# Kernel tuning notes

Hardware: AMD Instinct MI355X
Metric: run time of the kernel (lower is better)

Reference implementation:

```python
import jax, jax.numpy as jnp
import numpy as np

HEAD = 64            # RWKV_HEAD_SIZE
C = 1024             # n_embd = dim_att
F = 4096             # dim_ffn
B, T = 8, 256
H = C // HEAD
N_LAYER, LAYER_ID = 12, 1
GN_EPS = 1e-5 * 8 ** 2   # GroupNorm eps = 1e-5 * head_size_divisor^2


def bshift(x):
    """bidirectional_shift_multihead: per head, first half of channels shifted
    forward in time (right), second half shifted backward (left), zero-padded."""
    b, t, c = x.shape
    x4 = x.reshape(b, t, c // HEAD, HEAD)
    mid = HEAD // 2
    f = jnp.pad(x4[:, :-1, :, :mid], ((0, 0), (1, 0), (0, 0), (0, 0)))
    r = jnp.pad(x4[:, 1:, :, mid:], ((0, 0), (0, 1), (0, 0), (0, 0)))
    return jnp.concatenate([f, r], -1).reshape(b, t, c)


def layernorm(x, g, b):
    m = jnp.mean(x, -1, keepdims=True)
    v = jnp.mean((x - m) ** 2, -1, keepdims=True)
    return (x - m) * jax.lax.rsqrt(v + 1e-5) * g + b


def groupnorm(x, g, b):
    bb, t, c = x.shape
    xg = x.reshape(bb, t, H, HEAD)
    m = jnp.mean(xg, -1, keepdims=True)
    v = jnp.mean((xg - m) ** 2, -1, keepdims=True)
    return ((xg - m) * jax.lax.rsqrt(v + GN_EPS)).reshape(bb, t, c) * g + b


def wkv6_bi(r, k, v, w, u):
    """Bidirectional WKV6. r,k,v,w: [B,T,H,N]; u: [H,N].
    y_t = r_t . (S^fwd_t + u*k_t v_t^T + S^bwd_t), with per-channel decay
    d_t = exp(-exp(w_t)) applied to the state after each step in each direction."""
    d = jnp.exp(-jnp.exp(w))
    rT, kT, vT, dT = (jnp.moveaxis(a, 1, 0) for a in (r, k, v, d))  # [T,B,H,N]
    S0 = jnp.zeros((B, H, HEAD, HEAD), r.dtype)
    uB = u[None]  # [1,H,N]

    def fstep(S, inp):
        rt, kt, vt, dt = inp
        kv = kt[..., None] * vt[..., None, :]              # [B,H,N,N]
        y = jnp.einsum('bhj,bhji->bhi', rt, S + uB[..., None] * kv)
        return dt[..., None] * S + kv, y

    _, yf = jax.lax.scan(fstep, S0, (rT, kT, vT, dT))

    def bstep(S, inp):
        rt, kt, vt, dt = inp
        y = jnp.einsum('bhj,bhji->bhi', rt, S)
        return dt[..., None] * S + kt[..., None] * vt[..., None, :], y

    _, yb = jax.lax.scan(bstep, S0, (rT, kT, vT, dT), reverse=True)
    return jnp.moveaxis(yf + yb, 0, 1)  # [B,T,H,N]


def block_forward(x, ln1_g, ln1_b, ln2_g, ln2_b,
                  maa_x, maa_w, maa_k, maa_v, maa_r, maa_g, maa_w1, maa_w2,
                  time_decay, tdw1, tdw2, u, Wr, Wk, Wv, Wg, Wo, lnx_g, lnx_b,
                  cmaa_k, cmaa_r, Wck, Wcv, Wcr):
    # ---- RWKV_Tmix_V6 (attention) branch ----
    xa = layernorm(x, ln1_g, ln1_b)
    xx = bshift(xa) - xa
    a = jnp.tanh((xa + xx * maa_x) @ maa_w1).reshape(B, T, 5, -1)   # [B,T,5,32]
    m = jnp.einsum('btfd,fdc->fbtc', a, maa_w2)                      # [5,B,T,C]
    xw = xa + xx * (maa_w + m[0])
    xk = xa + xx * (maa_k + m[1])
    xv = xa + xx * (maa_v + m[2])
    xr = xa + xx * (maa_r + m[3])
    xg = xa + xx * (maa_g + m[4])
    r = (xr @ Wr).reshape(B, T, H, HEAD)
    k = (xk @ Wk).reshape(B, T, H, HEAD)
    v = (xv @ Wv).reshape(B, T, H, HEAD)
    g = jax.nn.silu(xg @ Wg)
    w = (time_decay + jnp.tanh(xw @ tdw1) @ tdw2).reshape(B, T, H, HEAD)
    y = wkv6_bi(r, k, v, w, u).reshape(B, T, C)
    y = groupnorm(y, lnx_g, lnx_b)
    x = x + (y * g) @ Wo
    # ---- RWKV_CMix_V6 (FFN) branch ----
    xc = layernorm(x, ln2_g, ln2_b)
    cxx = bshift(xc) - xc
    kk = jnp.square(jax.nn.relu((xc + cxx * cmaa_k) @ Wck))
    kv = kk @ Wcv
    x = x + jax.nn.sigmoid((xc + cxx * cmaa_r) @ Wcr) * kv
    return x


def setup_inputs() -> dict:
    key = jax.random.key(0)
    ks = jax.random.split(key, 16)
    r1 = 1.0 - LAYER_ID / N_LAYER            # ratio_1_to_almost0
    r0 = LAYER_ID / (N_LAYER - 1)            # ratio_0_to_1
    ddd = np.arange(C, dtype=np.float64) / C
    base = (1.0 - ddd ** r1).astype(np.float32)
    half = (1.0 - ddd ** (0.5 * r1)).astype(np.float32)
    s = 0.02
    p = {}
    p['x'] = jax.random.normal(ks[0], (B, T, C), jnp.float32)
    p['ln1_g'] = jnp.ones((C,), jnp.float32)
    p['ln1_b'] = jnp.zeros((C,), jnp.float32)
    p['ln2_g'] = jnp.ones((C,), jnp.float32)
    p['ln2_b'] = jnp.zeros((C,), jnp.float32)
    p['maa_x'] = jnp.asarray(base)
    p['maa_w'] = jnp.asarray(base)
    p['maa_k'] = jnp.asarray(base)
    p['maa_v'] = jnp.asarray((1.0 - (ddd ** r1 + 0.3 * r0)).astype(np.float32))
    p['maa_r'] = jnp.asarray(half)
    p['maa_g'] = jnp.asarray(half)
    p['maa_w1'] = jax.random.uniform(ks[1], (C, 160), jnp.float32, -0.01, 0.01)
    p['maa_w2'] = jax.random.uniform(ks[2], (5, 32, C), jnp.float32, -0.01, 0.01)
    n = np.arange(C, dtype=np.float64)
    p['time_decay'] = jnp.asarray((-6.0 + 5.0 * (n / (C - 1)) ** (0.7 + 1.3 * r0)).astype(np.float32))
    p['tdw1'] = jax.random.uniform(ks[3], (C, 64), jnp.float32, -0.01, 0.01)
    p['tdw2'] = jax.random.uniform(ks[4], (64, C), jnp.float32, -0.01, 0.01)
    faaaa = r0 * (1.0 - n / (C - 1)) + ((n + 1) % 3 - 1) * 0.1
    p['u'] = jnp.asarray(faaaa.reshape(H, HEAD).astype(np.float32))
    p['Wr'] = jax.random.normal(ks[5], (C, C), jnp.float32) * s
    p['Wk'] = jax.random.normal(ks[6], (C, C), jnp.float32) * s
    p['Wv'] = jax.random.normal(ks[7], (C, C), jnp.float32) * s
    p['Wg'] = jax.random.normal(ks[8], (C, C), jnp.float32) * s
    p['Wo'] = jax.random.normal(ks[9], (C, C), jnp.float32) * s
    p['lnx_g'] = jnp.ones((C,), jnp.float32)
    p['lnx_b'] = jnp.zeros((C,), jnp.float32)
    p['cmaa_k'] = jnp.asarray(base)
    p['cmaa_r'] = jnp.asarray(base)
    p['Wck'] = jax.random.normal(ks[10], (C, F), jnp.float32) * s
    p['Wcv'] = jax.random.normal(ks[11], (F, C), jnp.float32) * s
    p['Wcr'] = jax.random.normal(ks[12], (C, C), jnp.float32) * s
    return p


def reference(x, ln1_g, ln1_b, ln2_g, ln2_b,
              maa_x, maa_w, maa_k, maa_v, maa_r, maa_g, maa_w1, maa_w2,
              time_decay, tdw1, tdw2, u, Wr, Wk, Wv, Wg, Wo, lnx_g, lnx_b,
              cmaa_k, cmaa_r, Wck, Wcv, Wcr):
    return block_forward(x, ln1_g, ln1_b, ln2_g, ln2_b,
                         maa_x, maa_w, maa_k, maa_v, maa_r, maa_g, maa_w1, maa_w2,
                         time_decay, tdw1, tdw2, u, Wr, Wk, Wv, Wg, Wo, lnx_g, lnx_b,
                         cmaa_k, cmaa_r, Wck, Wcv, Wcr)
```

## Files before the change

### kernel.cpp

```cpp
#include <hip/hip_runtime.h>
#include <math.h>
#include <stdint.h>

static constexpr int B  = 8;
static constexpr int T  = 256;
static constexpr int C  = 1024;
static constexpr int H  = 16;
static constexpr int HEAD = 64;
static constexpr int FF = 4096;
static constexpr int BT = B * T;
static constexpr int NCH = 8;
static constexpr int CS  = 32;

typedef short short8  __attribute__((ext_vector_type(8)));
typedef float floatx4 __attribute__((ext_vector_type(4)));

__device__ __forceinline__ float bf2f(ushort u) {
    return __uint_as_float(((uint32_t)u) << 16);
}
__device__ __forceinline__ ushort f2bf(float x) {
    uint32_t u = __float_as_uint(x);
    u += 0x7fff + ((u >> 16) & 1);
    return (ushort)(u >> 16);
}

__device__ __forceinline__ void gload16(const void* g, void* l) {
    __builtin_amdgcn_global_load_lds(
        (const __attribute__((address_space(1))) unsigned int*)g,
        (__attribute__((address_space(3))) unsigned int*)l, 16, 0, 0);
}

#define BEPI_NONE_BF   0
#define BEPI_SILU_BF   1
#define BEPI_RELUSQ_BF 2
#define BEPI_NONE_F    3
#define BEPI_RES_F     4
#define BEPI_SIGRES_F  5
#define BEPI_TANH_F    6
#define BEPI_TANH_BF   7
#define BEPI_DECAY_F   8
#define BEPI_SIGRES2_F 9

__global__ __launch_bounds__(256) void ln_kernel(const float* __restrict__ x,
                                                 const float* __restrict__ g,
                                                 const float* __restrict__ b,
                                                 float* __restrict__ out)
{
    const int row = blockIdx.x;
    const int tid = threadIdx.x;
    const float4 v = reinterpret_cast<const float4*>(x + (size_t)row * C)[tid];
    float s = v.x + v.y + v.z + v.w;
#pragma unroll
    for (int off = 32; off > 0; off >>= 1) s += __shfl_xor(s, off);
    __shared__ float red[8];
    const int wave = tid >> 6, lane = tid & 63;
    if (lane == 0) red[wave] = s;
    __syncthreads();
    const float mean = (red[0] + red[1] + red[2] + red[3]) * (1.0f / C);
    const float d0 = v.x - mean, d1 = v.y - mean, d2 = v.z - mean, d3 = v.w - mean;
    float q = d0 * d0 + d1 * d1 + d2 * d2 + d3 * d3;
#pragma unroll
    for (int off = 32; off > 0; off >>= 1) q += __shfl_xor(q, off);
    if (lane == 0) red[4 + wave] = q;
    __syncthreads();
    const float var = (red[4] + red[5] + red[6] + red[7]) * (1.0f / C);
    const float rstd = rsqrtf(var + 1e-5f);
    const int c = tid * 4;
    float4 o;
    o.x = d0 * rstd * g[c + 0] + b[c + 0];
    o.y = d1 * rstd * g[c + 1] + b[c + 1];
    o.z = d2 * rstd * g[c + 2] + b[c + 2];
    o.w = d3 * rstd * g[c + 3] + b[c + 3];
    reinterpret_cast<float4*>(out + (size_t)row * C)[tid] = o;
}

__global__ __launch_bounds__(256) void bshiftmix_kernel(const float* __restrict__ xa,
                                                        const float* __restrict__ maa,
                                                        float* __restrict__ xx,
                                                        ushort* __restrict__ ax)
{
    const int i = blockIdx.x * 256 + threadIdx.x;
    const int c = i & (C - 1);
    const int bt = i >> 10;
    const int t = bt & (T - 1);
    const int j = c & (HEAD - 1);
    float src = 0.f;
    if (j < HEAD / 2) { if (t > 0)     src = xa[i - C]; }
    else              { if (t < T - 1) src = xa[i + C]; }
    const float a = xa[i];
    const float xv = src - a;
    xx[i] = xv;
    ax[i] = f2bf(a + xv * maa[c]);
}

__global__ __launch_bounds__(256) void bshiftcmix_kernel(const float* __restrict__ xc,
                                                         const float* __restrict__ mk,
                                                         const float* __restrict__ mr,
                                                         ushort* __restrict__ ok,
                                                         ushort* __restrict__ orr)
{
    const int i = blockIdx.x * 256 + threadIdx.x;
    const int c = i & (C - 1);
    const int bt = i >> 10;
    const int t = bt & (T - 1);
    const int j = c & (HEAD - 1);
    float src = 0.f;
    if (j < HEAD / 2) { if (t > 0)     src = xc[i - C]; }
    else              { if (t < T - 1) src = xc[i + C]; }
    const float a = xc[i];
    const float cxx = src - a;
    ok[i]  = f2bf(a + cxx * mk[c]);
    orr[i] = f2bf(a + cxx * mr[c]);
}

__global__ __launch_bounds__(1024) void gnmul_kernel(const float* __restrict__ yf,
                                                     const float* __restrict__ yb,
                                                     const float* __restrict__ g,
                                                     const float* __restrict__ b,
                                                     const ushort* __restrict__ gate,
                                                     const ushort* __restrict__ vin,
                                                     const ushort* __restrict__ rbuf,
                                                     const ushort* __restrict__ kbuf,
                                                     const float* __restrict__ u,
                                                     ushort* __restrict__ out)
{
    const int row = blockIdx.x;
    const int tid = threadIdx.x;
    const size_t idx = (size_t)row * C + tid;
    float p = bf2f(rbuf[idx]) * bf2f(kbuf[idx]) * u[tid];
#pragma unroll
    for (int off = 32; off > 0; off >>= 1) p += __shfl_xor(p, off);
    const float v = yf[idx] + yb[idx] + p * bf2f(vin[idx]);
    float s = v;
#pragma unroll
    for (int off = 32; off > 0; off >>= 1) s += __shfl_xor(s, off);
    const float m = s * (1.0f / HEAD);
    const float d = v - m;
    float q = d * d;
#pragma unroll
    for (int off = 32; off > 0; off >>= 1) q += __shfl_xor(q, off);
    const float rstd = rsqrtf(q * (1.0f / HEAD) + 6.4e-4f);
    out[idx] = f2bf((d * rstd * g[tid] + b[tid]) * bf2f(gate[idx]));
}

__global__ __launch_bounds__(256) void wconv_kernel(const float* __restrict__ W,
                                                    ushort* __restrict__ Wt,
                                                    int Kd, int Nd)
{
    __shared__ float tile[32][33];
    const int n0 = blockIdx.x * 32, k0 = blockIdx.y * 32;
    const int tx = threadIdx.x, ty = threadIdx.y;
#pragma unroll
    for (int i = 0; i < 4; ++i)
        tile[ty * 4 + i][tx] = W[(size_t)(k0 + ty * 4 + i) * Nd + n0 + tx];
    __syncthreads();
#pragma unroll
    for (int i = 0; i < 4; ++i)
        Wt[(size_t)(n0 + ty * 4 + i) * Kd + k0 + tx] = f2bf(tile[tx][ty * 4 + i]);
}

__global__ __launch_bounds__(256) void w2conv_kernel(const float* __restrict__ w2,
                                                     ushort* __restrict__ w2t)
{
    __shared__ float tile[32][33];
    const int f = blockIdx.y;
    const int n0 = blockIdx.x * 32;
    const int tx = threadIdx.x, ty = threadIdx.y;
#pragma unroll
    for (int i = 0; i < 4; ++i)
        tile[ty * 4 + i][tx] = w2[(size_t)f * 32 * C + (size_t)(ty * 4 + i) * C + n0 + tx];
    __syncthreads();
#pragma unroll
    for (int i = 0; i < 4; ++i)
        w2t[(size_t)f * C * 32 + (size_t)(n0 + ty * 4 + i) * 32 + tx] = f2bf(tile[tx][ty * 4 + i]);
}

struct Wconv4Args { const float* W[4]; };
__global__ __launch_bounds__(256) void wconv4_kernel(Wconv4Args args, ushort* __restrict__ Wt)
{
    __shared__ float tile[32][33];
    const int z = blockIdx.z;
    const float* __restrict__ W = args.W[z];
    ushort* __restrict__ dst = Wt + (size_t)z * C * C;
    const int n0 = blockIdx.x * 32, k0 = blockIdx.y * 32;
    const int tx = threadIdx.x, ty = threadIdx.y;
#pragma unroll
    for (int i = 0; i < 4; ++i)
        tile[ty * 4 + i][tx] = W[(size_t)(k0 + ty * 4 + i) * C + n0 + tx];
    __syncthreads();
#pragma unroll
    for (int i = 0; i < 4; ++i)
        dst[(size_t)(n0 + ty * 4 + i) * C + k0 + tx] = f2bf(tile[tx][ty * 4 + i]);
}

struct Mix5Args { const float* maa[5]; ushort* out[5]; };
__global__ __launch_bounds__(256) void mix5m_kernel(const ushort* __restrict__ a5b,
                                                    const ushort* __restrict__ w2t,
                                                    const float* __restrict__ xa,
                                                    const float* __restrict__ xx,
                                                    Mix5Args args)
{
    __shared__ __align__(16) ushort As[128 * 32];
    __shared__ __align__(16) ushort Bs[64 * 32];
    const int f = blockIdx.z;
    const int bm = blockIdx.y * 128, bn = blockIdx.x * 64;
    const int tid = threadIdx.x;
    const int wid = tid >> 6, lane = tid & 63;
    const int wr = wid >> 1, wc = wid & 1;
    const int l15 = lane & 15, lhi = lane >> 4;

#pragma unroll
    for (int p = 0; p < 2; ++p) {
        const int lin = p * 256 + tid;
        const int row = lin >> 2;
        const int sp = (lin & 3) ^ ((row >> 1) & 3);
        gload16(a5b + (size_t)(bm + row) * 160 + f * 32 + sp * 8, &As[lin * 8]);
    }
    {
        const int lin = tid;
        const int n = lin >> 2;
        const int sp = (lin & 3) ^ ((n >> 1) & 3);
        gload16(w2t + ((size_t)f * C + bn + n) * 32 + sp * 8, &Bs[lin * 8]);
    }
    __syncthreads();

    short8 af[4], bfr[2];
#pragma unroll
    for (int m = 0; m < 4; ++m) {
        const int row = wr * 64 + m * 16 + l15;
        const int sp = lhi ^ ((row >> 1) & 3);
        af[m] = *(const short8*)&As[row * 32 + sp * 8];
    }
#pragma unroll
    for (int n = 0; n < 2; ++n) {
        const int col = wc * 32 + n * 16 + l15;
        const int sp = lhi ^ ((col >> 1) & 3);
        bfr[n] = *(const short8*)&Bs[col * 32 + sp * 8];
    }
    floatx4 acc[4][2];
#pragma unroll
    for (int m = 0; m < 4; ++m)
#pragma unroll
        for (int n = 0; n < 2; ++n)
            acc[m][n] = __builtin_amdgcn_mfma_f32_16x16x32_bf16(
                af[m], bfr[n], (floatx4){0.f, 0.f, 0.f, 0.f}, 0, 0, 0);

    const float* __restrict__ maa = args.maa[f];
    ushort* __restrict__ out = args.out[f];
#pragma unroll
    for (int m = 0; m < 4; ++m) {
        const int row0 = bm + wr * 64 + m * 16 + lhi * 4;
#pragma unroll
        for (int n = 0; n < 2; ++n) {
            const int col = bn + wc * 32 + n * 16 + l15;
            const float mc = maa[col];
#pragma unroll
            for (int j = 0; j < 4; ++j) {
                const size_t oi = (size_t)(row0 + j) * C + col;
                out[oi] = f2bf(xa[oi] + xx[oi] * (mc + acc[m][n][j]));
            }
        }
    }
}

__global__ __launch_bounds__(256) void wkv_pass1(const ushort* __restrict__ k,
                                                 const ushort* __restrict__ v,
                                                 const float* __restrict__ d,
                                                 ushort* __restrict__ M,
                                                 float* __restrict__ D)
{
    const int uc = blockIdx.x;
    const int c = uc & (NCH - 1), unit = uc >> 3;
    const int dir = unit & 1, bh = unit >> 1;
    const int tid = threadIdx.x;
    const int wv = tid >> 6, lane = tid & 63;
    const int l15 = lane & 15, lhi = lane >> 4;
    const size_t rowb = ((size_t)(bh >> 4) * T * H + (bh & 15)) * HEAD;
    const int s0 = c * CS;

    __shared__ ushort kT[64][40];
    __shared__ ushort vt[64][40];
    __shared__ float  Ldd[CS][64];

    for (int idx = tid; idx < CS * 64; idx += 256) {
        const int s = idx >> 6, j = idx & 63;
        const int t = dir ? (T - 1 - (s0 + s)) : (s0 + s);
        const size_t g = rowb + (size_t)t * (H * HEAD) + j;
        kT[j][s] = k[g];
        vt[j][s] = v[g];
        Ldd[s][j] = d[g];
    }
    __syncthreads();

    if (tid < 64) {
        const int j = tid;
        float G = 1.f;
#pragma unroll
        for (int s = CS - 1; s >= 0; --s) {
            kT[j][s] = f2bf(bf2f(kT[j][s]) * G);
            G *= Ldd[s][j];
        }
        D[(size_t)uc * 64 + j] = G;
    }
    __syncthreads();

    const short8 av = *(const short8*)&vt[wv * 16 + l15][lhi * 8];
    ushort* __restrict__ mrow = M + (size_t)uc * 4096;
#pragma unroll
    for (int n = 0; n < 4; ++n) {
        const short8 bk = *(const short8*)&kT[n * 16 + l15][lhi * 8];
        const floatx4 acc = __builtin_amdgcn_mfma_f32_16x16x32_bf16(
            av, bk, (floatx4){0.f, 0.f, 0.f, 0.f}, 0, 0, 0);
#pragma unroll
        for (int jr = 0; jr < 4; ++jr) {
            const int i = wv * 16 + lhi * 4 + jr;
            mrow[(size_t)i * 64 + n * 16 + l15] = f2bf(acc[jr]);
        }
    }
}

__global__ __launch_bounds__(1024) void wkv_pass2(ushort* __restrict__ M,
                                                  const float* __restrict__ D)
{
    const int unit = blockIdx.x;
    const int tid = threadIdx.x;
    const int j0 = (tid & 15) * 4;
    float S0 = 0.f, S1 = 0.f, S2 = 0.f, S3 = 0.f;
#pragma unroll
    for (int c = 0; c < NCH; ++c) {
        const int uc = unit * NCH + c;
        const float4 Dv = *reinterpret_cast<const float4*>(D + (size_t)uc * 64 + j0);
        ushort* mp = M + (size_t)uc * 4096 + tid * 4;
        const uint2 mv = *reinterpret_cast<const uint2*>(mp);
        const float m0 = bf2f((ushort)(mv.x & 0xffff));
        const float m1 = bf2f((ushort)(mv.x >> 16));
        const float m2 = bf2f((ushort)(mv.y & 0xffff));
        const float m3 = bf2f((ushort)(mv.y >> 16));
        uint2 sv;
        sv.x = (uint32_t)f2bf(S0) | ((uint32_t)f2bf(S1) << 16);
        sv.y = (uint32_t)f2bf(S2) | ((uint32_t)f2bf(S3) << 16);
        *reinterpret_cast<uint2*>(mp) = sv;
        S0 = fmaf(Dv.x, S0, m0);
        S1 = fmaf(Dv.y, S1, m1);
        S2 = fmaf(Dv.z, S2, m2);
        S3 = fmaf(Dv.w, S3, m3);
    }
}

__global__ __launch_bounds__(256) void wkv_ymfma(const ushort* __restrict__ r,
                                                 const ushort* __restrict__ k,
                                                 const ushort* __restrict__ v,
                                                 const float* __restrict__ d,
                                                 const ushort* __restrict__ Sin,
                                                 float* __restrict__ yf,
                                                 float* __restrict__ yb)
{
    const int uc = blockIdx.x;
    const int c = uc & (NCH - 1), unit = uc >> 3;
    const int dir = unit & 1, bh = unit >> 1;
    const int tid = threadIdx.x;
    const int wv = tid >> 6, lane = tid & 63;
    const int l15 = lane & 15, lhi = lane >> 4;
    const size_t rowb = ((size_t)(bh >> 4) * T * H + (bh & 15)) * HEAD;
    const int s0 = c * CS;

    __shared__ ushort rp[32][64];
    __shared__ ushort kp[32][64];
    __shared__ ushort vt[64][40];
    __shared__ ushort Pl[32][32];
    __shared__ float  Ldd[CS][64];

    for (int idx = tid; idx < 32 * 64; idx += 256) {
        const int s = idx >> 6, j = idx & 63;
        const int t = dir ? (T - 1 - (s0 + s)) : (s0 + s);
        const size_t g = rowb + (size_t)t * (H * HEAD) + j;
        const int cs = (j >> 3) ^ (s & 7);
        rp[s][cs * 8 + (j & 7)] = r[g];
        kp[s][cs * 8 + (j & 7)] = k[g];
        vt[j][s] = v[g];
        Ldd[s][j] = d[g];
    }
    __syncthreads();

    if (wv == 0) {
        const int j = lane;
        float Q = 1.f;
#pragma unroll
        for (int s = 0; s < 32; ++s) {
            const int a = ((j >> 3) ^ (s & 7)) * 8 + (j & 7);
            rp[s][a] = f2bf(bf2f(rp[s][a]) * Q);
            Q *= Ldd[s][j];
        }
    } else if (wv == 1) {
        const int j = lane;
        float iQ = 1.f;
#pragma unroll
        for (int s = 0; s < 32; ++s) {
            iQ *= (1.0f / Ldd[s][j]);
            const int a = ((j >> 3) ^ (s & 7)) * 8 + (j & 7);
            kp[s][a] = f2bf(bf2f(kp[s][a]) * iQ);
        }
    }
    __syncthreads();

    const int st = wv & 1;
    const int ip = wv >> 1;

    short8 ar[2];
#pragma unroll
    for (int ks = 0; ks < 2; ++ks) {
        const int row = st * 16 + l15;
        const int ch = (ks * 4 + lhi) ^ (row & 7);
        ar[ks] = *(const short8*)&rp[row][ch * 8];
    }

    floatx4 acc[2];
#pragma unroll
    for (int n = 0; n < 2; ++n) {
        const int i = ip * 32 + n * 16 + l15;
        const ushort* sp = Sin + (size_t)uc * 4096 + (size_t)i * 64;
        const short8 b0 = *(const short8*)&sp[lhi * 8];
        const short8 b1 = *(const short8*)&sp[32 + lhi * 8];
        acc[n] = __builtin_amdgcn_mfma_f32_16x16x32_bf16(ar[0], b0, (floatx4){0.f, 0.f, 0.f, 0.f}, 0, 0, 0);
        acc[n] = __builtin_amdgcn_mfma_f32_16x16x32_bf16(ar[1], b1, acc[n], 0, 0, 0);
    }

    if (wv < 2) {
#pragma unroll
        for (int ut = 0; ut < 2; ++ut) {
            const int urow = ut * 16 + l15;
            const short8 bk0 = *(const short8*)&kp[urow][((0 + lhi) ^ (urow & 7)) * 8];
            const short8 bk1 = *(const short8*)&kp[urow][((4 + lhi) ^ (urow & 7)) * 8];
            floatx4 pa = __builtin_amdgcn_mfma_f32_16x16x32_bf16(ar[0], bk0, (floatx4){0.f, 0.f, 0.f, 0.f}, 0, 0, 0);
            pa = __builtin_amdgcn_mfma_f32_16x16x32_bf16(ar[1], bk1, pa, 0, 0, 0);
            const int sg0 = st * 16 + lhi * 4;
            const int ug = ut * 16 + l15;
#pragma unroll
            for (int jr = 0; jr < 4; ++jr) {
                const float val = (ug < sg0 + jr) ? pa[jr] : 0.f;
                Pl[sg0 + jr][ug] = f2bf(val);
            }
        }
    }
    __syncthreads();

    short8 ap;
    {
        const int row = st * 16 + l15;
        ap = *(const short8*)&Pl[row][lhi * 8];
    }
#pragma unroll
    for (int n = 0; n < 2; ++n) {
        const int i = ip * 32 + n * 16 + l15;
        const short8 bv = *(const short8*)&vt[i][lhi * 8];
        acc[n] = __builtin_amdgcn_mfma_f32_16x16x32_bf16(ap, bv, acc[n], 0, 0, 0);
    }

    float* __restrict__ yo = dir ? yb : yf;
#pragma unroll
    for (int n = 0; n < 2; ++n) {
        const int i = ip * 32 + n * 16 + l15;
#pragma unroll
        for (int jr = 0; jr < 4; ++jr) {
            const int sg = st * 16 + lhi * 4 + jr;
            const int t = dir ? (T - 1 - (s0 + sg)) : (s0 + sg);
            yo[rowb + (size_t)t * (H * HEAD) + i] = acc[n][jr];
        }
    }
}

template <int BN>
struct GemmLds {
    ushort As[2][128 * 64];
    ushort Bs[2][BN * 64];
};

template <int BN>
__device__ __forceinline__ void gemm_body(const ushort* __restrict__ A,
                                          const ushort* __restrict__ Bt,
                                          int bm, int bn, int K, int lda, int ldb,
                                          GemmLds<BN>& lds,
                                          floatx4 (&acc)[4][BN / 32])
{
    constexpr int NF = BN / 32;
    const int tid = threadIdx.x;
    const int wid = tid >> 6, lane = tid & 63;
    const int wr = wid >> 1, wc = wid & 1;
    const int l15 = lane & 15, lhi = lane >> 4;
    const int NT = K >> 6;

    auto stage = [&](int buf, int k0) {
#pragma unroll
        for (int p = 0; p < 4; ++p) {
            const int lin = p * 256 + tid;
            const int row = lin >> 3;
            const int cs = (lin & 7) ^ (row & 7);
            gload16(A + (size_t)(bm + row) * lda + k0 + cs * 8, &lds.As[buf][lin * 8]);
        }
#pragma unroll
        for (int p = 0; p < NF; ++p) {
            const int lin = p * 256 + tid;
            const int n = lin >> 3;
            const int cs = (lin & 7) ^ (n & 7);
            gload16(Bt + (size_t)(bn + n) * ldb + k0 + cs * 8, &lds.Bs[buf][lin * 8]);
        }
    };

    stage(0, 0);
    __syncthreads();
    for (int t = 0; t < NT; ++t) {
        const int cur = t & 1;
        if (t + 1 < NT) stage(cur ^ 1, (t + 1) << 6);

        short8 af[4][2];
#pragma unroll
        for (int m = 0; m < 4; ++m) {
            const int row = wr * 64 + m * 16 + l15;
#pragma unroll
            for (int s = 0; s < 2; ++s) {
                const int cc = (s * 4 + lhi) ^ (row & 7);
                af[m][s] = *(const short8*)&lds.As[cur][row * 64 + cc * 8];
            }
        }
        short8 bf[NF][2];
#pragma unroll
        for (int n = 0; n < NF; ++n) {
            const int col = wc * (BN / 2) + n * 16 + l15;
#pragma unroll
            for (int s = 0; s < 2; ++s) {
                const int cc = (s * 4 + lhi) ^ (col & 7);
                bf[n][s] = *(const short8*)&lds.Bs[cur][col * 64 + cc * 8];
            }
        }
#pragma unroll
        for (int m = 0; m < 4; ++m)
#pragma unroll
            for (int n = 0; n < NF; ++n) {
                acc[m][n] = __builtin_amdgcn_mfma_f32_16x16x32_bf16(af[m][0], bf[n][0], acc[m][n], 0, 0, 0);
                acc[m][n] = __builtin_amdgcn_mfma_f32_16x16x32_bf16(af[m][1], bf[n][1], acc[m][n], 0, 0, 0);
            }
        __syncthreads();
    }
}

template <int BN, int EPI>
__global__ __launch_bounds__(256) void bgemm_kernel(const ushort* __restrict__ A,
                                                    const ushort* __restrict__ Bt,
                                                    void* __restrict__ Cm,
                                                    int M, int N, int K,
                                                    const float* __restrict__ aux1,
                                                    const float* __restrict__ aux2,
                                                    const float* __restrict__ aux3)
{
    constexpr int NF = BN / 32;
    __shared__ GemmLds<BN> lds;
    int w = blockIdx.y * gridDim.x + blockIdx.x;
    const int nwg = gridDim.x * gridDim.y;
    if ((nwg & 7) == 0) w = (w & 7) * (nwg >> 3) + (w >> 3);
    const int bn = (w % gridDim.x) * BN;
    const int bm = (w / gridDim.x) * 128;
    const int tid = threadIdx.x;
    const int wid = tid >> 6, lane = tid & 63;
    const int wr = wid >> 1, wc = wid & 1;
    const int l15 = lane & 15, lhi = lane >> 4;

    floatx4 acc[4][NF];
#pragma unroll
    for (int m = 0; m < 4; ++m)
#pragma unroll
        for (int n = 0; n < NF; ++n) acc[m][n] = (floatx4){0.f, 0.f, 0.f, 0.f};

    gemm_body<BN>(A, Bt, bm, bn, K, K, K, lds, acc);

#pragma unroll
    for (int m = 0; m < 4; ++m) {
        const int row0 = bm + wr * 64 + m * 16 + lhi * 4;
#pragma unroll
        for (int n = 0; n < NF; ++n) {
            const int col = bn + wc * (BN / 2) + n * 16 + l15;
            if (col >= N) continue;
#pragma unroll
            for (int j = 0; j < 4; ++j) {
                const size_t oi = (size_t)(row0 + j) * N + col;
                const float a = acc[m][n][j];
                if constexpr (EPI == BEPI_NONE_BF) {
                    ((ushort*)Cm)[oi] = f2bf(a);
                } else if constexpr (EPI == BEPI_SILU_BF) {
                    ((ushort*)Cm)[oi] = f2bf(a / (1.f + __expf(-a)));
                } else if constexpr (EPI == BEPI_RELUSQ_BF) {
                    const float t = fmaxf(a, 0.f);
                    ((ushort*)Cm)[oi] = f2bf(t * t);
                } else if constexpr (EPI == BEPI_NONE_F) {
                    ((float*)Cm)[oi] = a;
                } else if constexpr (EPI == BEPI_RES_F) {
                    ((float*)Cm)[oi] = aux1[oi] + a;
                } else if constexpr (EPI == BEPI_SIGRES_F) {
                    ((float*)Cm)[oi] = aux1[oi] + aux2[oi] / (1.f + __expf(-a));
                } else if constexpr (EPI == BEPI_SIGRES2_F) {
                    ((float*)Cm)[oi] = aux1[oi] + (aux2[oi] + aux3[oi]) / (1.f + __expf(-a));
                } else if constexpr (EPI == BEPI_TANH_F) {
                    ((float*)Cm)[oi] = tanhf(a);
                } else if constexpr (EPI == BEPI_TANH_BF) {
                    ((ushort*)Cm)[oi] = f2bf(tanhf(a));
                } else {
                    ((float*)Cm)[oi] = __expf(-__expf(a + aux1[col]));
                }
            }
        }
    }
}

__global__ __launch_bounds__(256) void wcv_kernel(const ushort* __restrict__ A,
                                                  const ushort* __restrict__ Bt,
                                                  float* __restrict__ P0,
                                                  float* __restrict__ P1)
{
    __shared__ GemmLds<64> lds;
    const int z = blockIdx.z;
    int w = blockIdx.y * gridDim.x + blockIdx.x;
    w = (w & 7) * 32 + (w >> 3);
    const int bn = (w % 16) * 64;
    const int bm = (w / 16) * 128;
    const int tid = threadIdx.x;
    const int wid = tid >> 6, lane = tid & 63;
    const int wr = wid >> 1, wc = wid & 1;
    const int l15 = lane & 15, lhi = lane >> 4;

    floatx4 acc[4][2];
#pragma unroll
    for (int m = 0; m < 4; ++m)
#pragma unroll
        for (int n = 0; n < 2; ++n) acc[m][n] = (floatx4){0.f, 0.f, 0.f, 0.f};

    gemm_body<64>(A + z * (FF / 2), Bt + z * (FF / 2), bm, bn, FF / 2, FF, FF, lds, acc);

    float* __restrict__ P = z ? P1 : P0;
#pragma unroll
    for (int m = 0; m < 4; ++m) {
        const int row0 = bm + wr * 64 + m * 16 + lhi * 4;
#pragma unroll
        for (int n = 0; n < 2; ++n) {
            const int col = bn + wc * 32 + n * 16 + l15;
#pragma unroll
            for (int j = 0; j < 4; ++j)
                P[(size_t)(row0 + j) * C + col] = acc[m][n][j];
        }
    }
}

struct QkvgArgs { const ushort* A[4]; ushort* O[4]; };
__global__ __launch_bounds__(256) void qkvg_kernel(QkvgArgs args,
                                                   const ushort* __restrict__ Wt)
{
    __shared__ GemmLds<128> lds;
    const int z = blockIdx.z;
    int w = blockIdx.y * gridDim.x + blockIdx.x;
    w = (w & 7) * 16 + (w >> 3);
    const int bn = (w & 7) * 128;
    const int bm = (w >> 3) * 128;
    const int tid = threadIdx.x;
    const int wid = tid >> 6, lane = tid & 63;
    const int wr = wid >> 1, wc = wid & 1;
    const int l15 = lane & 15, lhi = lane >> 4;

    floatx4 acc[4][4];
#pragma unroll
    for (int m = 0; m < 4; ++m)
#pragma unroll
        for (int n = 0; n < 4; ++n) acc[m][n] = (floatx4){0.f, 0.f, 0.f, 0.f};

    gemm_body<128>(args.A[z], Wt + (size_t)z * C * C, bm, bn, C, C, C, lds, acc);

    ushort* __restrict__ O = args.O[z];
    const bool silu = (z == 3);
#pragma unroll
    for (int m = 0; m < 4; ++m) {
        const int row0 = bm + wr * 64 + m * 16 + lhi * 4;
#pragma unroll
        for (int n = 0; n < 4; ++n) {
            const int col = bn + wc * 64 + n * 16 + l15;
#pragma unroll
            for (int j = 0; j < 4; ++j) {
                float a = acc[m][n][j];
                if (silu) a = a / (1.f + __expf(-a));
                O[(size_t)(row0 + j) * C + col] = f2bf(a);
            }
        }
    }
}

extern "C" void kernel_launch(void* const* d_in, const int* in_sizes, int n_in,
                              void* d_out, int out_size, void* d_ws, size_t ws_size,
                              hipStream_t stream)
{
    const float* x        = (const float*)d_in[0];
    const float* ln1_g    = (const float*)d_in[1];
    const float* ln1_b    = (const float*)d_in[2];
    const float* ln2_g    = (const float*)d_in[3];
    const float* ln2_b    = (const float*)d_in[4];
    const float* maa_x    = (const float*)d_in[5];
    const float* maa_w    = (const float*)d_in[6];
    const float* maa_k    = (const float*)d_in[7];
    const float* maa_v    = (const float*)d_in[8];
    const float* maa_r    = (const float*)d_in[9];
    const float* maa_g    = (const float*)d_in[10];
    const float* maa_w1   = (const float*)d_in[11];
    const float* maa_w2   = (const float*)d_in[12];
    const float* time_dec = (const float*)d_in[13];
    const float* tdw1     = (const float*)d_in[14];
    const float* tdw2     = (const float*)d_in[15];
    const float* u        = (const float*)d_in[16];
    const float* Wr       = (const float*)d_in[17];
    const float* Wk       = (const float*)d_in[18];
    const float* Wv       = (const float*)d_in[19];
    const float* Wg       = (const float*)d_in[20];
    const float* Wo       = (const float*)d_in[21];
    const float* lnx_g    = (const float*)d_in[22];
    const float* lnx_b    = (const float*)d_in[23];
    const float* cmaa_k   = (const float*)d_in[24];
    const float* cmaa_r   = (const float*)d_in[25];
    const float* Wck      = (const float*)d_in[26];
    const float* Wcv      = (const float*)d_in[27];
    const float* Wcr      = (const float*)d_in[28];
    float* out = (float*)d_out;

    float* fws = (float*)d_ws;
    const size_t E = (size_t)BT * C;
    float* xa  = fws + 0 * E;
    float* xx  = fws + 1 * E;
    float* wd  = fws + 2 * E;
    float* fs  = fws + 3 * E;
    ushort* wBuf = (ushort*)(fws + 4 * E);
    ushort* Mbuf = (ushort*)fs;
    ushort* w2t  = wBuf + (size_t)C * 160;
    ushort* bf1  = wBuf + (size_t)C * FF;
    ushort* rb   = bf1 + E;
    ushort* kb   = rb + E;
    ushort* vb   = kb + E;
    ushort* gb   = vb + E;
    ushort* t1b  = gb + E;
    float* a5    = (float*)(t1b + (size_t)BT * 64);
    float* sig   = a5 + (size_t)BT * 160;
    float* Dbuf  = sig + (size_t)BT * H;
    ushort* a5b  = (ushort*)a5;
    ushort* xvb  = (ushort*)fs;
    ushort* xrb  = (ushort*)fs + E;
    ushort* xgb  = (ushort*)out;
    ushort* xwb  = (ushort*)out + E;
    ushort* kk   = (ushort*)xa;

    const dim3 blk(256);
    const dim3 tblk(32, 8);
    const int EW = (BT * C) / 256;
    const dim3 gNN(C / 64, BT / 128);

    ln_kernel<<<BT, blk, 0, stream>>>(x, ln1_g, ln1_b, xa);
    bshiftmix_kernel<<<EW, blk, 0, stream>>>(xa, maa_x, xx, bf1);
    wconv_kernel<<<dim3(160 / 32, C / 32), tblk, 0, stream>>>(maa_w1, wBuf, C, 160);
    bgemm_kernel<64, BEPI_TANH_BF><<<dim3(3, BT / 128), blk, 0, stream>>>(bf1, wBuf, a5b, BT, 160, C, nullptr, nullptr, nullptr);

    w2conv_kernel<<<dim3(C / 32, 5), tblk, 0, stream>>>(maa_w2, w2t);

    Mix5Args margs;
    margs.maa[0] = maa_w; margs.maa[1] = maa_k; margs.maa[2] = maa_v;
    margs.maa[3] = maa_r; margs.maa[4] = maa_g;
    margs.out[0] = xwb; margs.out[1] = bf1; margs.out[2] = xvb;
    margs.out[3] = xrb; margs.out[4] = xgb;
    mix5m_kernel<<<dim3(C / 64, BT / 128, 5), blk, 0, stream>>>(a5b, w2t, xa, xx, margs);

    wconv_kernel<<<dim3(64 / 32, C / 32), tblk, 0, stream>>>(tdw1, wBuf, C, 64);
    bgemm_kernel<64, BEPI_TANH_BF><<<dim3(1, BT / 128), blk, 0, stream>>>(xwb, wBuf, t1b, BT, 64, C, nullptr, nullptr, nullptr);
    wconv_kernel<<<dim3(C / 32, 64 / 32), tblk, 0, stream>>>(tdw2, wBuf, 64, C);
    bgemm_kernel<64, BEPI_DECAY_F><<<gNN, blk, 0, stream>>>(t1b, wBuf, wd, BT, C, 64, time_dec, nullptr, nullptr);

    Wconv4Args wargs;
    wargs.W[0] = Wk; wargs.W[1] = Wv; wargs.W[2] = Wr; wargs.W[3] = Wg;
    wconv4_kernel<<<dim3(C / 32, C / 32, 4), tblk, 0, stream>>>(wargs, wBuf);
    QkvgArgs qargs;
    qargs.A[0] = bf1; qargs.A[1] = xvb; qargs.A[2] = xrb; qargs.A[3] = xgb;
    qargs.O[0] = kb;  qargs.O[1] = vb;  qargs.O[2] = rb;  qargs.O[3] = gb;
    qkvg_kernel<<<dim3(8, 16, 4), blk, 0, stream>>>(qargs, wBuf);

    wkv_pass1<<<dim3(2 * B * H * NCH), blk, 0, stream>>>(kb, vb, wd, Mbuf, Dbuf);
    wkv_pass2<<<dim3(2 * B * H), dim3(1024), 0, stream>>>(Mbuf, Dbuf);
    wkv_ymfma<<<dim3(2 * B * H * NCH), blk, 0, stream>>>(rb, kb, vb, wd, Mbuf, xa, xx);

    gnmul_kernel<<<BT, dim3(1024), 0, stream>>>(xa, xx, lnx_g, lnx_b, gb, vb, rb, kb, u, vb);
    wconv_kernel<<<dim3(C / 32, C / 32), tblk, 0, stream>>>(Wo, wBuf, C, C);
    bgemm_kernel<64, BEPI_RES_F><<<gNN, blk, 0, stream>>>(vb, wBuf, out, BT, C, C, x, nullptr, nullptr);

    ln_kernel<<<BT, blk, 0, stream>>>(out, ln2_g, ln2_b, wd);
    bshiftcmix_kernel<<<EW, blk, 0, stream>>>(wd, cmaa_k, cmaa_r, bf1, gb);
    wconv_kernel<<<dim3(FF / 32, C / 32), tblk, 0, stream>>>(Wck, wBuf, C, FF);
    bgemm_kernel<128, BEPI_RELUSQ_BF><<<dim3(FF / 128, BT / 128), blk, 0, stream>>>(bf1, wBuf, kk, BT, FF, C, nullptr, nullptr, nullptr);
    wconv_kernel<<<dim3(C / 32, FF / 32), tblk, 0, stream>>>(Wcv, wBuf, FF, C);
    wcv_kernel<<<dim3(16, 16, 2), blk, 0, stream>>>(kk, wBuf, fs, wd);
    wconv_kernel<<<dim3(C / 32, C / 32), tblk, 0, stream>>>(Wcr, wBuf, C, C);
    bgemm_kernel<64, BEPI_SIGRES2_F><<<gNN, blk, 0, stream>>>(gb, wBuf, out, BT, C, C, out, fs, wd);

    (void)in_sizes; (void)n_in; (void)out_size; (void)ws_size;
}
```

Measured before the change: 255.6 us.

## Fuse layernorm with bidirectional shift-mix and store intermediates in bf16

Merges each layernorm with the following shift/mix elementwise kernel. Each row block recomputes the layernorm statistics of its neighbouring rows, so the normalized tensor no longer has to be written out and read back. The statistics switch to a single-pass sum and sum-of-squares form. Separately, the WKV forward/backward outputs and the split-K FFN partial sums are stored as bf16 instead of fp32, halving that memory traffic. The trade-offs are triple row loads in the fused kernel and reduced precision in intermediates.

```diff
diff --git a/kernel.cpp b/kernel.cpp
--- a/kernel.cpp
+++ b/kernel.cpp
@@ -41,80 +41,125 @@
 #define BEPI_DECAY_F   8
 #define BEPI_SIGRES2_F 9
 
-__global__ __launch_bounds__(256) void ln_kernel(const float* __restrict__ x,
-                                                 const float* __restrict__ g,
-                                                 const float* __restrict__ b,
-                                                 float* __restrict__ out)
+__device__ __forceinline__ void red6(float (&vals)[6], float* red)
+{
+    const int wave = threadIdx.x >> 6, lane = threadIdx.x & 63;
+#pragma unroll
+    for (int i = 0; i < 6; ++i) {
+        float v = vals[i];
+#pragma unroll
+        for (int off = 32; off > 0; off >>= 1) v += __shfl_xor(v, off);
+        if (lane == 0) red[i * 4 + wave] = v;
+    }
+    __syncthreads();
+#pragma unroll
+    for (int i = 0; i < 6; ++i)
+        vals[i] = red[i * 4 + 0] + red[i * 4 + 1] + red[i * 4 + 2] + red[i * 4 + 3];
+}
+
+__global__ __launch_bounds__(256) void lnshiftmix_kernel(const float* __restrict__ x,
+                                                         const float* __restrict__ g,
+                                                         const float* __restrict__ b,
+                                                         const float* __restrict__ maa,
+                                                         float* __restrict__ xa,
+                                                         float* __restrict__ xx,
+                                                         ushort* __restrict__ ax)
 {
     const int row = blockIdx.x;
-    const int tid = threadIdx.x;
-    const float4 v = reinterpret_cast<const float4*>(x + (size_t)row * C)[tid];
-    float s = v.x + v.y + v.z + v.w;
-#pragma unroll
-    for (int off = 32; off > 0; off >>= 1) s += __shfl_xor(s, off);
-    __shared__ float red[8];
-    const int wave = tid >> 6, lane = tid & 63;
-    if (lane == 0) red[wave] = s;
-    __syncthreads();
-    const float mean = (red[0] + red[1] + red[2] + red[3]) * (1.0f / C);
-    const float d0 = v.x - mean, d1 = v.y - mean, d2 = v.z - mean, d3 = v.w - mean;
-    float q = d0 * d0 + d1 * d1 + d2 * d2 + d3 * d3;
-#pragma unroll
-    for (int off = 32; off > 0; off >>= 1) q += __shfl_xor(q, off);
-    if (lane == 0) red[4 + wave] = q;
-    __syncthreads();
-    const float var = (red[4] + red[5] + red[6] + red[7]) * (1.0f / C);
-    const float rstd = rsqrtf(var + 1e-5f);
+    const int t = row & (T - 1);
+    const int tid = threadIdx.x;
+    __shared__ float red[24];
+    const float4 vc = reinterpret_cast<const float4*>(x + (size_t)row * C)[tid];
+    float4 vp = make_float4(0.f, 0.f, 0.f, 0.f), vn = make_float4(0.f, 0.f, 0.f, 0.f);
+    if (t > 0)     vp = reinterpret_cast<const float4*>(x + (size_t)(row - 1) * C)[tid];
+    if (t < T - 1) vn = reinterpret_cast<const float4*>(x + (size_t)(row + 1) * C)[tid];
+    float vals[6];
+    vals[0] = vc.x + vc.y + vc.z + vc.w;
+    vals[1] = vc.x * vc.x + vc.y * vc.y + vc.z * vc.z + vc.w * vc.w;
+    vals[2] = vp.x + vp.y + vp.z + vp.w;
+    vals[3] = vp.x * vp.x + vp.y * vp.y + vp.z * vp.z + vp.w * vp.w;
+    vals[4] = vn.x + vn.y + vn.z + vn.w;
+    vals[5] = vn.x * vn.x + vn.y * vn.y + vn.z * vn.z + vn.w * vn.w;
+    red6(vals, red);
+    const float mc = vals[0] * (1.f / C);
+    const float rc = rsqrtf(fmaxf(vals[1] * (1.f / C) - mc * mc, 0.f) + 1e-5f);
+    const float mp = vals[2] * (1.f / C);
+    const float rp = rsqrtf(fmaxf(vals[3] * (1.f / C) - mp * mp, 0.f) + 1e-5f);
+    const float mn = vals[4] * (1.f / C);
+    const float rn = rsqrtf(fmaxf(vals[5] * (1.f / C) - mn * mn, 0.f) + 1e-5f);
+
     const int c = tid * 4;
-    float4 o;
-    o.x = d0 * rstd * g[c + 0] + b[c + 0];
-    o.y = d1 * rstd * g[c + 1] + b[c + 1];
-    o.z = d2 * rstd * g[c + 2] + b[c + 2];
-    o.w = d3 * rstd * g[c + 3] + b[c + 3];
-    reinterpret_cast<float4*>(out + (size_t)row * C)[tid] = o;
-}
-
-__global__ __launch_bounds__(256) void bshiftmix_kernel(const float* __restrict__ xa,
-                                                        const float* __restrict__ maa,
-                                                        float* __restrict__ xx,
-                                                        ushort* __restrict__ ax)
-{
-    const int i = blockIdx.x * 256 + threadIdx.x;
-    const int c = i & (C - 1);
-    const int bt = i >> 10;
-    const int t = bt & (T - 1);
-    const int j = c & (HEAD - 1);
-    float src = 0.f;
-    if (j < HEAD / 2) { if (t > 0)     src = xa[i - C]; }
-    else              { if (t < T - 1) src = xa[i + C]; }
-    const float a = xa[i];
-    const float xv = src - a;
-    xx[i] = xv;
-    ax[i] = f2bf(a + xv * maa[c]);
-}
-
-__global__ __launch_bounds__(256) void bshiftcmix_kernel(const float* __restrict__ xc,
-                                                         const float* __restrict__ mk,
-                                                         const float* __restrict__ mr,
-                                                         ushort* __restrict__ ok,
-                                                         ushort* __restrict__ orr)
-{
-    const int i = blockIdx.x * 256 + threadIdx.x;
-    const int c = i & (C - 1);
-    const int bt = i >> 10;
-    const int t = bt & (T - 1);
-    const int j = c & (HEAD - 1);
-    float src = 0.f;
-    if (j < HEAD / 2) { if (t > 0)     src = xc[i - C]; }
-    else              { if (t < T - 1) src = xc[i + C]; }
-    const float a = xc[i];
-    const float cxx = src - a;
-    ok[i]  = f2bf(a + cxx * mk[c]);
-    orr[i] = f2bf(a + cxx * mr[c]);
-}
-
-__global__ __launch_bounds__(1024) void gnmul_kernel(const float* __restrict__ yf,
-                                                     const float* __restrict__ yb,
+    const bool fh = ((c & 63) < 32);
+    const float cur[4] = {vc.x, vc.y, vc.z, vc.w};
+    const float nbr[4] = {fh ? vp.x : vn.x, fh ? vp.y : vn.y,
+                          fh ? vp.z : vn.z, fh ? vp.w : vn.w};
+    const float mN = fh ? mp : mn, rN = fh ? rp : rn;
+    const bool nvalid = fh ? (t > 0) : (t < T - 1);
+    const size_t rb = (size_t)row * C;
+#pragma unroll
+    for (int e = 0; e < 4; ++e) {
+        const float gg = g[c + e], bb = b[c + e];
+        const float av = (cur[e] - mc) * rc * gg + bb;
+        const float sv = nvalid ? ((nbr[e] - mN) * rN * gg + bb) : 0.f;
+        const float xv = sv - av;
+        xa[rb + c + e] = av;
+        xx[rb + c + e] = xv;
+        ax[rb + c + e] = f2bf(av + xv * maa[c + e]);
+    }
+}
+
+__global__ __launch_bounds__(256) void lnshiftcmix_kernel(const float* __restrict__ x,
+                                                          const float* __restrict__ g,
+                                                          const float* __restrict__ b,
+                                                          const float* __restrict__ mk,
+                                                          const float* __restrict__ mr,
+                                                          ushort* __restrict__ ok,
+                                                          ushort* __restrict__ orr)
+{
+    const int row = blockIdx.x;
+    const int t = row & (T - 1);
+    const int tid = threadIdx.x;
+    __shared__ float red[24];
+    const float4 vc = reinterpret_cast<const float4*>(x + (size_t)row * C)[tid];
+    float4 vp = make_float4(0.f, 0.f, 0.f, 0.f), vn = make_float4(0.f, 0.f, 0.f, 0.f);
+    if (t > 0)     vp = reinterpret_cast<const float4*>(x + (size_t)(row - 1) * C)[tid];
+    if (t < T - 1) vn = reinterpret_cast<const float4*>(x + (size_t)(row + 1) * C)[tid];
+    float vals[6];
+    vals[0] = vc.x + vc.y + vc.z + vc.w;
+    vals[1] = vc.x * vc.x + vc.y * vc.y + vc.z * vc.z + vc.w * vc.w;
+    vals[2] = vp.x + vp.y + vp.z + vp.w;
+    vals[3] = vp.x * vp.x + vp.y * vp.y + vp.z * vp.z + vp.w * vp.w;
+    vals[4] = vn.x + vn.y + vn.z + vn.w;
+    vals[5] = vn.x * vn.x + vn.y * vn.y + vn.z * vn.z + vn.w * vn.w;
+    red6(vals, red);
+    const float mc = vals[0] * (1.f / C);
+    const float rc = rsqrtf(fmaxf(vals[1] * (1.f / C) - mc * mc, 0.f) + 1e-5f);
+    const float mp = vals[2] * (1.f / C);
+    const float rp = rsqrtf(fmaxf(vals[3] * (1.f / C) - mp * mp, 0.f) + 1e-5f);
+    const float mn = vals[4] * (1.f / C);
+    const float rn = rsqrtf(fmaxf(vals[5] * (1.f / C) - mn * mn, 0.f) + 1e-5f);
+
+    const int c = tid * 4;
+    const bool fh = ((c & 63) < 32);
+    const float cur[4] = {vc.x, vc.y, vc.z, vc.w};
+    const float nbr[4] = {fh ? vp.x : vn.x, fh ? vp.y : vn.y,
+                          fh ? vp.z : vn.z, fh ? vp.w : vn.w};
+    const float mN = fh ? mp : mn, rN = fh ? rp : rn;
+    const bool nvalid = fh ? (t > 0) : (t < T - 1);
+    const size_t rb = (size_t)row * C;
+#pragma unroll
+    for (int e = 0; e < 4; ++e) {
+        const float gg = g[c + e], bb = b[c + e];
+        const float av = (cur[e] - mc) * rc * gg + bb;
+        const float sv = nvalid ? ((nbr[e] - mN) * rN * gg + bb) : 0.f;
+        const float xv = sv - av;
+        ok[rb + c + e]  = f2bf(av + xv * mk[c + e]);
+        orr[rb + c + e] = f2bf(av + xv * mr[c + e]);
+    }
+}
+
+__global__ __launch_bounds__(1024) void gnmul_kernel(const ushort* __restrict__ yf,
+                                                     const ushort* __restrict__ yb,
                                                      const float* __restrict__ g,
                                                      const float* __restrict__ b,
                                                      const ushort* __restrict__ gate,
@@ -130,7 +175,7 @@
     float p = bf2f(rbuf[idx]) * bf2f(kbuf[idx]) * u[tid];
 #pragma unroll
     for (int off = 32; off > 0; off >>= 1) p += __shfl_xor(p, off);
-    const float v = yf[idx] + yb[idx] + p * bf2f(vin[idx]);
+    const float v = bf2f(yf[idx]) + bf2f(yb[idx]) + p * bf2f(vin[idx]);
     float s = v;
 #pragma unroll
     for (int off = 32; off > 0; off >>= 1) s += __shfl_xor(s, off);
@@ -352,8 +397,8 @@
                                                  const ushort* __restrict__ v,
                                                  const float* __restrict__ d,
                                                  const ushort* __restrict__ Sin,
-                                                 float* __restrict__ yf,
-                                                 float* __restrict__ yb)
+                                                 ushort* __restrict__ yf,
+                                                 ushort* __restrict__ yb)
 {
     const int uc = blockIdx.x;
     const int c = uc & (NCH - 1), unit = uc >> 3;
@@ -456,7 +501,7 @@
         acc[n] = __builtin_amdgcn_mfma_f32_16x16x32_bf16(ap, bv, acc[n], 0, 0, 0);
     }
 
-    float* __restrict__ yo = dir ? yb : yf;
+    ushort* __restrict__ yo = dir ? yb : yf;
 #pragma unroll
     for (int n = 0; n < 2; ++n) {
         const int i = ip * 32 + n * 16 + l15;
@@ -464,7 +509,7 @@
         for (int jr = 0; jr < 4; ++jr) {
             const int sg = st * 16 + lhi * 4 + jr;
             const int t = dir ? (T - 1 - (s0 + sg)) : (s0 + sg);
-            yo[rowb + (size_t)t * (H * HEAD) + i] = acc[n][jr];
+            yo[rowb + (size_t)t * (H * HEAD) + i] = f2bf(acc[n][jr]);
         }
     }
 }
@@ -597,7 +642,9 @@
                 } else if constexpr (EPI == BEPI_SIGRES_F) {
                     ((float*)Cm)[oi] = aux1[oi] + aux2[oi] / (1.f + __expf(-a));
                 } else if constexpr (EPI == BEPI_SIGRES2_F) {
-                    ((float*)Cm)[oi] = aux1[oi] + (aux2[oi] + aux3[oi]) / (1.f + __expf(-a));
+                    const float kv = bf2f(((const ushort*)aux2)[oi]) +
+                                     bf2f(((const ushort*)aux3)[oi]);
+                    ((float*)Cm)[oi] = aux1[oi] + kv / (1.f + __expf(-a));
                 } else if constexpr (EPI == BEPI_TANH_F) {
                     ((float*)Cm)[oi] = tanhf(a);
                 } else if constexpr (EPI == BEPI_TANH_BF) {
@@ -612,8 +659,8 @@
 
 __global__ __launch_bounds__(256) void wcv_kernel(const ushort* __restrict__ A,
                                                   const ushort* __restrict__ Bt,
-                                                  float* __restrict__ P0,
-                                                  float* __restrict__ P1)
+                                                  ushort* __restrict__ P0,
+                                                  ushort* __restrict__ P1)
 {
     __shared__ GemmLds<64> lds;
     const int z = blockIdx.z;
@@ -634,7 +681,7 @@
 
     gemm_body<64>(A + z * (FF / 2), Bt + z * (FF / 2), bm, bn, FF / 2, FF, FF, lds, acc);
 
-    float* __restrict__ P = z ? P1 : P0;
+    ushort* __restrict__ P = z ? P1 : P0;
 #pragma unroll
     for (int m = 0; m < 4; ++m) {
         const int row0 = bm + wr * 64 + m * 16 + lhi * 4;
@@ -643,7 +690,7 @@
             const int col = bn + wc * 32 + n * 16 + l15;
 #pragma unroll
             for (int j = 0; j < 4; ++j)
-                P[(size_t)(row0 + j) * C + col] = acc[m][n][j];
+                P[(size_t)(row0 + j) * C + col] = f2bf(acc[m][n][j]);
         }
     }
 }
@@ -747,15 +794,17 @@
     ushort* xrb  = (ushort*)fs + E;
     ushort* xgb  = (ushort*)out;
     ushort* xwb  = (ushort*)out + E;
+    ushort* yfb  = (ushort*)xa;
+    ushort* ybb  = (ushort*)xa + E;
+    ushort* p0b  = (ushort*)fs;
+    ushort* p1b  = (ushort*)fs + E;
     ushort* kk   = (ushort*)xa;
 
     const dim3 blk(256);
     const dim3 tblk(32, 8);
-    const int EW = (BT * C) / 256;
     const dim3 gNN(C / 64, BT / 128);
 
-    ln_kernel<<<BT, blk, 0, stream>>>(x, ln1_g, ln1_b, xa);
-    bshiftmix_kernel<<<EW, blk, 0, stream>>>(xa, maa_x, xx, bf1);
+    lnshiftmix_kernel<<<BT, blk, 0, stream>>>(x, ln1_g, ln1_b, maa_x, xa, xx, bf1);
     wconv_kernel<<<dim3(160 / 32, C / 32), tblk, 0, stream>>>(maa_w1, wBuf, C, 160);
     bgemm_kernel<64, BEPI_TANH_BF><<<dim3(3, BT / 128), blk, 0, stream>>>(bf1, wBuf, a5b, BT, 160, C, nullptr, nullptr, nullptr);
 
@@ -783,20 +832,19 @@
 
     wkv_pass1<<<dim3(2 * B * H * NCH), blk, 0, stream>>>(kb, vb, wd, Mbuf, Dbuf);
     wkv_pass2<<<dim3(2 * B * H), dim3(1024), 0, stream>>>(Mbuf, Dbuf);
-    wkv_ymfma<<<dim3(2 * B * H * NCH), blk, 0, stream>>>(rb, kb, vb, wd, Mbuf, xa, xx);
-
-    gnmul_kernel<<<BT, dim3(1024), 0, stream>>>(xa, xx, lnx_g, lnx_b, gb, vb, rb, kb, u, vb);
+    wkv_ymfma<<<dim3(2 * B * H * NCH), blk, 0, stream>>>(rb, kb, vb, wd, Mbuf, yfb, ybb);
+
+    gnmul_kernel<<<BT, dim3(1024), 0, stream>>>(yfb, ybb, lnx_g, lnx_b, gb, vb, rb, kb, u, vb);
     wconv_kernel<<<dim3(C / 32, C / 32), tblk, 0, stream>>>(Wo, wBuf, C, C);
     bgemm_kernel<64, BEPI_RES_F><<<gNN, blk, 0, stream>>>(vb, wBuf, out, BT, C, C, x, nullptr, nullptr);
 
-    ln_kernel<<<BT, blk, 0, stream>>>(out, ln2_g, ln2_b, wd);
-    bshiftcmix_kernel<<<EW, blk, 0, stream>>>(wd, cmaa_k, cmaa_r, bf1, gb);
+    lnshiftcmix_kernel<<<BT, blk, 0, stream>>>(out, ln2_g, ln2_b, cmaa_k, cmaa_r, bf1, gb);
     wconv_kernel<<<dim3(FF / 32, C / 32), tblk, 0, stream>>>(Wck, wBuf, C, FF);
     bgemm_kernel<128, BEPI_RELUSQ_BF><<<dim3(FF / 128, BT / 128), blk, 0, stream>>>(bf1, wBuf, kk, BT, FF, C, nullptr, nullptr, nullptr);
     wconv_kernel<<<dim3(C / 32, FF / 32), tblk, 0, stream>>>(Wcv, wBuf, FF, C);
-    wcv_kernel<<<dim3(16, 16, 2), blk, 0, stream>>>(kk, wBuf, fs, wd);
+    wcv_kernel<<<dim3(16, 16, 2), blk, 0, stream>>>(kk, wBuf, p0b, p1b);
     wconv_kernel<<<dim3(C / 32, C / 32), tblk, 0, stream>>>(Wcr, wBuf, C, C);
-    bgemm_kernel<64, BEPI_SIGRES2_F><<<gNN, blk, 0, stream>>>(gb, wBuf, out, BT, C, C, out, fs, wd);
+    bgemm_kernel<64, BEPI_SIGRES2_F><<<gNN, blk, 0, stream>>>(gb, wBuf, out, BT, C, C, out, (const float*)p0b, (const float*)p1b);
 
     (void)in_sizes; (void)n_in; (void)out_size; (void)ws_size;
 }
```

Result: no change. 251.3 us (-1.7%).
